# Performance work log

Hardware: AMD Instinct MI355X
Metric: run time of the kernel (lower is better)

## Reference

```python
import jax, jax.numpy as jnp
import numpy as np

N_U, N_P, E = 200000, 50000, 500000
D_U, D_P, H, OUT = 100, 50, 128, 1
BN_EPS = 1e-5


def _lin(k, dout, din):
    s = 1.0 / np.sqrt(din)
    kw, kb = jax.random.split(k)
    W = jax.random.uniform(kw, (dout, din), jnp.float32, -s, s)
    b = jax.random.uniform(kb, (dout,), jnp.float32, -s, s)
    return W, b


def setup_inputs() -> dict:
    key = jax.random.key(0)
    ks = jax.random.split(key, 12)
    x_u = jax.random.normal(ks[0], (N_U, D_U), jnp.float32)
    x_p = jax.random.normal(ks[1], (N_P, D_P), jnp.float32)
    src = jax.random.randint(ks[2], (E,), 0, N_U, jnp.int64) if jax.config.jax_enable_x64 else jax.random.randint(ks[2], (E,), 0, N_U)
    dst = jax.random.randint(ks[3], (E,), N_U, N_U + N_P)
    edge_index = jnp.stack([src, dst]).astype(jnp.int32)
    W_u, b_u = _lin(ks[4], H, D_U)
    W_p, b_p = _lin(ks[5], H, D_P)
    W1l, b1l = _lin(ks[6], H, H)   # SAGEConv lin_l (aggregated neighbors, carries bias)
    W1r, _ = _lin(ks[7], H, H)     # SAGEConv lin_r (root, no bias)
    W2l, b2l = _lin(ks[8], H, H)
    W2r, _ = _lin(ks[9], H, H)
    W_out, b_out = _lin(ks[10], OUT, H)
    return dict(x_u=x_u, x_p=x_p, edge_index=edge_index,
                W_u=W_u, b_u=b_u, W_p=W_p, b_p=b_p,
                W1l=W1l, b1l=b1l, W1r=W1r,
                g1=jnp.ones((H,), jnp.float32), be1=jnp.zeros((H,), jnp.float32),
                W2l=W2l, b2l=b2l, W2r=W2r,
                g2=jnp.ones((H,), jnp.float32), be2=jnp.zeros((H,), jnp.float32),
                W_out=W_out, b_out=b_out)


def reference(x_u, x_p, edge_index, W_u, b_u, W_p, b_p,
              W1l, b1l, W1r, g1, be1, W2l, b2l, W2r, g2, be2,
              W_out, b_out):
    N = x_u.shape[0] + x_p.shape[0]
    # input projections + relu, then concat users/products -> [N, H]
    x = jnp.concatenate([jax.nn.relu(x_u @ W_u.T + b_u),
                         jax.nn.relu(x_p @ W_p.T + b_p)], axis=0)
    # to_undirected: add reversed edges (bipartite => no duplicates)
    src = jnp.concatenate([edge_index[0], edge_index[1]])
    dst = jnp.concatenate([edge_index[1], edge_index[0]])
    deg = jnp.maximum(jax.ops.segment_sum(jnp.ones_like(dst, jnp.float32), dst, num_segments=N), 1.0)

    def sage(h, Wl, bl, Wr):
        # mean aggregation of neighbor features, scatter by dst
        mean = jax.ops.segment_sum(h[src], dst, num_segments=N) / deg[:, None]
        return mean @ Wl.T + bl + h @ Wr.T

    def bn(h, g, b):
        m = h.mean(0)
        v = h.var(0)  # biased variance, as used for normalization in torch BN
        return (h - m) * jax.lax.rsqrt(v + BN_EPS) * g + b

    h1 = jax.nn.relu(bn(sage(x, W1l, b1l, W1r), g1, be1))   # dropout = identity (eval)
    h2 = jax.nn.relu(bn(sage(h1, W2l, b2l, W2r), g2, be2)) + x
    return h2[: x_u.shape[0]] @ W_out.T + b_out
```

## Files before the change

### kernel.cpp

```cpp
#include <hip/hip_runtime.h>
#include <hip/hip_bf16.h>
#include <cstdint>
#include <cstddef>

#define NT   250000
#define NUU  200000
#define NPP  50000
#define EG   500000
#define E2   1000000
#define HD   128
#define NBLK_SCAN 977

#define CNT2_OFF   0ull
#define SPART2_OFF 1000000ull
#define SS2_OFF    1065536ull
#define RPTR2_OFF  1067584ull
#define BSUM2_OFF  2067588ull
#define BMAT2_OFF  2071504ull
#define COL2_OFF   2251728ull
#define X2_OFF     6251728ull
#define R1B_OFF    70251728ull
#define R2B_OFF    134251728ull
#define WS_SPLIT   198251728ull

typedef __hip_bfloat16 bf16;
typedef __attribute__((ext_vector_type(8))) short short8v;
typedef __attribute__((ext_vector_type(4))) float f32x4;

__device__ inline float b2f(short s) { return __builtin_bit_cast(float, ((unsigned)(unsigned short)s) << 16); }
__device__ inline unsigned short f2bf(float f) { return __builtin_bit_cast(unsigned short, __float2bfloat16(f)); }

__global__ __launch_bounds__(256) void k_zero(int* __restrict__ p, int n) {
    for (int i = blockIdx.x * 256 + threadIdx.x; i < n; i += gridDim.x * 256) p[i] = 0;
}

__global__ __launch_bounds__(256) void k_count(const int* __restrict__ ei, int* __restrict__ cnt) {
    for (int e = blockIdx.x * 256 + threadIdx.x; e < E2; e += gridDim.x * 256) {
        int d = (e < EG) ? ei[e + EG] : ei[e - EG];
        atomicAdd(&cnt[d], 1);
    }
}

__global__ __launch_bounds__(256) void k_scan1(const int* __restrict__ cnt, int* __restrict__ bsum) {
    __shared__ int lds[256];
    int i = blockIdx.x * 256 + threadIdx.x;
    int v = (i < NT) ? cnt[i] : 0;
    lds[threadIdx.x] = v; __syncthreads();
    for (int s = 128; s > 0; s >>= 1) {
        if (threadIdx.x < s) lds[threadIdx.x] += lds[threadIdx.x + s];
        __syncthreads();
    }
    if (threadIdx.x == 0) bsum[blockIdx.x] = lds[0];
}

__global__ __launch_bounds__(1024) void k_scan2(int* __restrict__ bsum) {
    __shared__ int lds[1024];
    int i = threadIdx.x;
    int v = (i < NBLK_SCAN) ? bsum[i] : 0;
    lds[i] = v; __syncthreads();
    for (int off = 1; off < 1024; off <<= 1) {
        int t = (i >= off) ? lds[i - off] : 0;
        __syncthreads();
        lds[i] += t;
        __syncthreads();
    }
    if (i < NBLK_SCAN) bsum[i] = lds[i] - v;
}

__global__ __launch_bounds__(256) void k_scan3(const int* __restrict__ cnt, const int* __restrict__ bsum,
                                               int* __restrict__ rp) {
    __shared__ int lds[256];
    int i = blockIdx.x * 256 + threadIdx.x;
    int v = (i < NT) ? cnt[i] : 0;
    lds[threadIdx.x] = v; __syncthreads();
    for (int off = 1; off < 256; off <<= 1) {
        int t = (threadIdx.x >= off) ? lds[threadIdx.x - off] : 0;
        __syncthreads();
        lds[threadIdx.x] += t;
        __syncthreads();
    }
    if (i < NT) rp[i] = bsum[blockIdx.x] + lds[threadIdx.x] - v;
    if (i == 0 && blockIdx.x == 0) rp[NT] = E2;
}

__global__ __launch_bounds__(256) void k_fill(const int* __restrict__ ei, const int* __restrict__ rp,
                                              int* __restrict__ fill, int* __restrict__ col) {
    for (int e = blockIdx.x * 256 + threadIdx.x; e < E2; e += gridDim.x * 256) {
        int s = ei[e];
        int d = (e < EG) ? ei[e + EG] : ei[e - EG];
        int slot = rp[d] + atomicAdd(&fill[d], 1);
        col[slot] = s;
    }
}

__global__ __launch_bounds__(256) void k_wcvt(const float* __restrict__ W1l, const float* __restrict__ W1r,
                                              const float* __restrict__ W2l, const float* __restrict__ W2r,
                                              const float* __restrict__ Wu, const float* __restrict__ Wp,
                                              bf16* __restrict__ B) {
    int i = blockIdx.x * 256 + threadIdx.x;
    if (i < 65536) {
        int layer = i >> 15, rem = i & 32767, o = rem >> 8, k = rem & 255;
        const float* W = layer ? ((k < 128) ? W2l : W2r) : ((k < 128) ? W1l : W1r);
        B[i] = __float2bfloat16(W[o * 128 + (k & 127)]);
    } else if (i < 81920) {
        int rem = i - 65536, o = rem >> 7, k = rem & 127;
        B[i] = __float2bfloat16((k < 100) ? Wu[o * 100 + k] : 0.f);
    } else if (i < 90112) {
        int rem = i - 81920, o = rem >> 6, k = rem & 63;
        B[i] = __float2bfloat16((k < 50) ? Wp[o * 50 + k] : 0.f);
    }
}

template<int DIN, int KPAD>
__global__ __launch_bounds__(256) void k_projm(const float* __restrict__ in, const bf16* __restrict__ Bp,
                                               const float* __restrict__ bias, bf16* __restrict__ outp,
                                               int nrows, int rowbase) {
    __shared__ __align__(16) char As[128 * KPAD * 2];
    const int tid = threadIdx.x;
    const int tb = blockIdx.x * 128;
    constexpr int RSTRIDE = KPAD * 2;
    constexpr int PADE = KPAD - DIN;
    constexpr int PH = PADE / 2;
    constexpr int PPAD = 128 * PH;
    constexpr int PMAIN = 128 * DIN / 2;

    for (int q = tid; q < PPAD; q += 256) {
        int row = q / PH;
        int k = DIN + (q - row * PH) * 2;
        *(unsigned*)(As + row * RSTRIDE + ((((k >> 3) << 4) ^ ((row & 7) << 4)) + (k & 7) * 2)) = 0u;
    }
    for (int q = tid; q < PMAIN; q += 256) {
        int f = q * 2;
        int row = f / DIN, k = f - row * DIN;
        int rg = tb + row; if (rg > nrows - 1) rg = nrows - 1;
        float2 v = *(const float2*)(in + (size_t)rg * DIN + k);
        unsigned u = (unsigned)f2bf(v.x) | ((unsigned)f2bf(v.y) << 16);
        *(unsigned*)(As + row * RSTRIDE + ((((k >> 3) << 4) ^ ((row & 7) << 4)) + (k & 7) * 2)) = u;
    }
    __syncthreads();

    const int lane = tid & 63, wid = tid >> 6;
    const int wr = wid >> 1, wc = wid & 1;
    const int r15 = lane & 15, l4 = lane >> 4;
    constexpr int NKS = KPAD / 32;
    f32x4 acc[4][4] = {};
#pragma unroll
    for (int ks = 0; ks < NKS; ks++) {
        short8v a[4], b[4];
#pragma unroll
        for (int m = 0; m < 4; m++) {
            int rl = wr * 64 + m * 16 + r15;
            a[m] = *(const short8v*)(As + rl * RSTRIDE + ((ks * 64 + l4 * 16) ^ ((rl & 7) << 4)));
        }
#pragma unroll
        for (int n = 0; n < 4; n++) {
            int c = wc * 64 + n * 16 + r15;
            b[n] = *(const short8v*)(Bp + (size_t)c * KPAD + ks * 32 + l4 * 8);
        }
#pragma unroll
        for (int m = 0; m < 4; m++)
#pragma unroll
            for (int n = 0; n < 4; n++)
                acc[m][n] = __builtin_amdgcn_mfma_f32_16x16x32_bf16(a[m], b[n], acc[m][n], 0, 0, 0);
    }
    float bcol[4];
#pragma unroll
    for (int n = 0; n < 4; n++) bcol[n] = bias[wc * 64 + n * 16 + r15];
#pragma unroll
    for (int m = 0; m < 4; m++)
#pragma unroll
        for (int n = 0; n < 4; n++)
#pragma unroll
            for (int g = 0; g < 4; g++) {
                int row = tb + wr * 64 + m * 16 + l4 * 4 + g;
                if (row < nrows) {
                    float v = fmaxf(acc[m][n][g] + bcol[n], 0.f);
                    outp[(size_t)(rowbase + row) * HD + wc * 64 + n * 16 + r15] = __float2bfloat16(v);
                }
            }
}

template<bool NORM>
__global__ __launch_bounds__(256) void k_layer(const bf16* __restrict__ hin, const float* __restrict__ ssv,
                                               const int* __restrict__ rp, const int* __restrict__ col,
                                               const bf16* __restrict__ Bmat, const float* __restrict__ blv,
                                               bf16* __restrict__ outp, float* __restrict__ spart,
                                               int store_n) {
    __shared__ __align__(16) char At[32768];
    __shared__ int rpl[129];
    __shared__ int ctr;
    const int tid = threadIdx.x;
    const int tb = blockIdx.x * 128;

    if (tid < 129) rpl[tid] = rp[min(tb + tid, NT)];
    if (tid == 255) ctr = 0;
    __syncthreads();

    const int lane = tid & 63;
    const int l8 = tid & 7;
    const int fo = l8 * 8;
    float sva[8], tva[8], svb[8], tvb[8];
    if (NORM) {
#pragma unroll
        for (int j = 0; j < 8; j++) {
            sva[j] = ssv[fo + j];      tva[j] = ssv[HD + fo + j];
            svb[j] = ssv[64 + fo + j]; tvb[j] = ssv[HD + 64 + fo + j];
        }
    }
    for (;;) {
        int nl = 0;
        if (l8 == 0) nl = atomicAdd(&ctr, 1);
        nl = __shfl(nl, lane & 56);
        if (nl >= 128) break;
        int s0 = rpl[nl], s1 = rpl[nl + 1];
        float a[8] = {}, b[8] = {};
        for (int p = s0; p < s1; p += 4) {
            int i1 = min(p + 1, s1 - 1), i2 = min(p + 2, s1 - 1), i3 = min(p + 3, s1 - 1);
            int c0 = col[p], c1 = col[i1], c2 = col[i2], c3 = col[i3];
            const bf16* r0p = hin + (size_t)c0 * HD + fo;
            const bf16* r1p = hin + (size_t)c1 * HD + fo;
            const bf16* r2p = hin + (size_t)c2 * HD + fo;
            const bf16* r3p = hin + (size_t)c3 * HD + fo;
            short8v uA0 = *(const short8v*)r0p, uB0 = *(const short8v*)(r0p + 64);
            short8v uA1 = *(const short8v*)r1p, uB1 = *(const short8v*)(r1p + 64);
            short8v uA2 = *(const short8v*)r2p, uB2 = *(const short8v*)(r2p + 64);
            short8v uA3 = *(const short8v*)r3p, uB3 = *(const short8v*)(r3p + 64);
            float m1 = (p + 1 < s1) ? 1.f : 0.f;
            float m2 = (p + 2 < s1) ? 1.f : 0.f;
            float m3 = (p + 3 < s1) ? 1.f : 0.f;
#pragma unroll
            for (int j = 0; j < 8; j++) {
                float vA0 = b2f(uA0[j]), vA1 = b2f(uA1[j]), vA2 = b2f(uA2[j]), vA3 = b2f(uA3[j]);
                float vB0 = b2f(uB0[j]), vB1 = b2f(uB1[j]), vB2 = b2f(uB2[j]), vB3 = b2f(uB3[j]);
                if (NORM) {
                    vA0 = fmaxf(fmaf(vA0, sva[j], tva[j]), 0.f);
                    vA1 = fmaxf(fmaf(vA1, sva[j], tva[j]), 0.f);
                    vA2 = fmaxf(fmaf(vA2, sva[j], tva[j]), 0.f);
                    vA3 = fmaxf(fmaf(vA3, sva[j], tva[j]), 0.f);
                    vB0 = fmaxf(fmaf(vB0, svb[j], tvb[j]), 0.f);
                    vB1 = fmaxf(fmaf(vB1, svb[j], tvb[j]), 0.f);
                    vB2 = fmaxf(fmaf(vB2, svb[j], tvb[j]), 0.f);
                    vB3 = fmaxf(fmaf(vB3, svb[j], tvb[j]), 0.f);
                }
                a[j] += vA0 + m1 * vA1 + m2 * vA2 + m3 * vA3;
                b[j] += vB0 + m1 * vB1 + m2 * vB2 + m3 * vB3;
            }
        }
        float inv = 1.f / (float)max(s1 - s0, 1);
        short8v wa, wb;
#pragma unroll
        for (int j = 0; j < 8; j++) { wa[j] = (short)f2bf(a[j] * inv); wb[j] = (short)f2bf(b[j] * inv); }
        *(short8v*)(At + nl * 256 + ((l8 * 16) ^ ((nl & 7) << 4))) = wa;
        *(short8v*)(At + nl * 256 + (((8 + l8) * 16) ^ ((nl & 7) << 4))) = wb;
    }

    const int seg = tid & 15, r0 = tid >> 4;
    const int sfo = seg * 8;
    short8v vh[8];
#pragma unroll
    for (int it = 0; it < 8; it++) {
        int row = r0 + it * 16;
        int r = tb + row; if (r > NT - 1) r = NT - 1;
        vh[it] = *(const short8v*)(hin + (size_t)r * HD + sfo);
    }
    __syncthreads();

    const int wid = tid >> 6;
    const int wr = wid >> 1, wc = wid & 1;
    const int r15 = lane & 15, l4 = lane >> 4;
    f32x4 acc[4][4] = {};
#pragma unroll
    for (int ks = 0; ks < 4; ks++) {
        short8v a[4], b[4];
#pragma unroll
        for (int m = 0; m < 4; m++) {
            int rl = wr * 64 + m * 16 + r15;
            a[m] = *(const short8v*)(At + rl * 256 + ((ks * 64 + l4 * 16) ^ ((rl & 7) << 4)));
        }
#pragma unroll
        for (int n = 0; n < 4; n++) {
            int c = wc * 64 + n * 16 + r15;
            b[n] = *(const short8v*)(Bmat + (size_t)c * 256 + ks * 32 + l4 * 8);
        }
#pragma unroll
        for (int m = 0; m < 4; m++)
#pragma unroll
            for (int n = 0; n < 4; n++)
                acc[m][n] = __builtin_amdgcn_mfma_f32_16x16x32_bf16(a[m], b[n], acc[m][n], 0, 0, 0);
    }
    __syncthreads();

    if (NORM) {
        float sv2[8], tv2[8];
#pragma unroll
        for (int j = 0; j < 8; j++) { sv2[j] = ssv[sfo + j]; tv2[j] = ssv[HD + sfo + j]; }
#pragma unroll
        for (int it = 0; it < 8; it++) {
#pragma unroll
            for (int j = 0; j < 8; j++) {
                float f = b2f(vh[it][j]);
                vh[it][j] = (short)f2bf(fmaxf(fmaf(f, sv2[j], tv2[j]), 0.f));
            }
        }
    }
#pragma unroll
    for (int it = 0; it < 8; it++) {
        int row = r0 + it * 16;
        *(short8v*)(At + row * 256 + ((seg * 16) ^ ((row & 7) << 4))) = vh[it];
    }
    __syncthreads();

#pragma unroll
    for (int ks = 0; ks < 4; ks++) {
        short8v a[4], b[4];
#pragma unroll
        for (int m = 0; m < 4; m++) {
            int rl = wr * 64 + m * 16 + r15;
            a[m] = *(const short8v*)(At + rl * 256 + ((ks * 64 + l4 * 16) ^ ((rl & 7) << 4)));
        }
#pragma unroll
        for (int n = 0; n < 4; n++) {
            int c = wc * 64 + n * 16 + r15;
            b[n] = *(const short8v*)(Bmat + (size_t)c * 256 + (ks + 4) * 32 + l4 * 8);
        }
#pragma unroll
        for (int m = 0; m < 4; m++)
#pragma unroll
            for (int n = 0; n < 4; n++)
                acc[m][n] = __builtin_amdgcn_mfma_f32_16x16x32_bf16(a[m], b[n], acc[m][n], 0, 0, 0);
    }

    float bcol[4];
#pragma unroll
    for (int n = 0; n < 4; n++) bcol[n] = blv[wc * 64 + n * 16 + r15];
    float ls[4] = {0.f, 0.f, 0.f, 0.f}, lq[4] = {0.f, 0.f, 0.f, 0.f};
#pragma unroll
    for (int m = 0; m < 4; m++)
#pragma unroll
        for (int n = 0; n < 4; n++)
#pragma unroll
            for (int gg = 0; gg < 4; gg++) {
                int row = tb + wr * 64 + m * 16 + l4 * 4 + gg;
                float v = acc[m][n][gg] + bcol[n];
                if (row < NT) { ls[n] += v; lq[n] += v * v; }
                if (row < store_n)
                    outp[(size_t)row * HD + wc * 64 + n * 16 + r15] = __float2bfloat16(v);
            }
    int part = (blockIdx.x & 31) * 256;
#pragma unroll
    for (int n = 0; n < 4; n++) {
        float s = ls[n], q2 = lq[n];
        s  += __shfl_xor(s, 16);  s  += __shfl_xor(s, 32);
        q2 += __shfl_xor(q2, 16); q2 += __shfl_xor(q2, 32);
        if (l4 == 0) {
            atomicAdd(&spart[part + wc * 64 + n * 16 + r15], s);
            atomicAdd(&spart[part + 128 + wc * 64 + n * 16 + r15], q2);
        }
    }
}

__global__ void k_fin(const float* __restrict__ sp, const float* __restrict__ g,
                      const float* __restrict__ be, float* __restrict__ ssout) {
    int j = threadIdx.x;
    float m = 0.f, q = 0.f;
    for (int i = 0; i < 32; i++) { m += sp[i * 256 + j]; q += sp[i * 256 + 128 + j]; }
    m *= (1.f / (float)NT);
    q = q * (1.f / (float)NT) - m * m;
    float s = g[j] * rsqrtf(q + 1e-5f);
    ssout[j] = s;
    ssout[HD + j] = be[j] - m * s;
}

__global__ __launch_bounds__(256) void k_out(const bf16* __restrict__ r2, const float* __restrict__ ss,
                                             const bf16* __restrict__ x, const float* __restrict__ wout,
                                             const float* __restrict__ bout, float* __restrict__ outp) {
    int lane = threadIdx.x & 63;
    int wv = (blockIdx.x * blockDim.x + threadIdx.x) >> 6;
    int nwv = (gridDim.x * blockDim.x) >> 6;
    int g16 = lane >> 4, l16 = lane & 15;
    int fo = l16 * 8;
    float s8[8], t8[8], w8[8];
#pragma unroll
    for (int j = 0; j < 8; j++) {
        s8[j] = ss[fo + j]; t8[j] = ss[HD + fo + j]; w8[j] = wout[fo + j];
    }
    float bo = bout[0];
    for (int r0 = wv * 4; r0 < NUU; r0 += nwv * 4) {
        int row = r0 + g16;
        short8v a  = *(const short8v*)(r2 + (size_t)row * HD + fo);
        short8v xx = *(const short8v*)(x  + (size_t)row * HD + fo);
        float acc = 0.f;
#pragma unroll
        for (int j = 0; j < 8; j++) {
            float h = fmaxf(fmaf(b2f(a[j]), s8[j], t8[j]), 0.f) + b2f(xx[j]);
            acc += h * w8[j];
        }
        acc += __shfl_xor(acc, 1);
        acc += __shfl_xor(acc, 2);
        acc += __shfl_xor(acc, 4);
        acc += __shfl_xor(acc, 8);
        if (l16 == 0) outp[row] = acc + bo;
    }
}

extern "C" void kernel_launch(void* const* d_in, const int* in_sizes, int n_in,
                              void* d_out, int out_size, void* d_ws, size_t ws_size,
                              hipStream_t stream) {
    const float* x_u = (const float*)d_in[0];
    const float* x_p = (const float*)d_in[1];
    const int*   ei  = (const int*)d_in[2];
    const float* W_u = (const float*)d_in[3];
    const float* b_u = (const float*)d_in[4];
    const float* W_p = (const float*)d_in[5];
    const float* b_p = (const float*)d_in[6];
    const float* W1l = (const float*)d_in[7];
    const float* b1l = (const float*)d_in[8];
    const float* W1r = (const float*)d_in[9];
    const float* g1  = (const float*)d_in[10];
    const float* be1 = (const float*)d_in[11];
    const float* W2l = (const float*)d_in[12];
    const float* b2l = (const float*)d_in[13];
    const float* W2r = (const float*)d_in[14];
    const float* g2  = (const float*)d_in[15];
    const float* be2 = (const float*)d_in[16];
    const float* Wout = (const float*)d_in[17];
    const float* bout = (const float*)d_in[18];
    float* out = (float*)d_out;
    char* ws = (char*)d_ws;

    if (ws_size < WS_SPLIT) {
        k_zero<<<512, 256, 0, stream>>>((int*)d_out, out_size);
        return;
    }

    int*  cnt    = (int*)(ws + CNT2_OFF);
    float* spart = (float*)(ws + SPART2_OFF);
    float* ssbuf = (float*)(ws + SS2_OFF);
    int*  rp     = (int*)(ws + RPTR2_OFF);
    int*  bsum   = (int*)(ws + BSUM2_OFF);
    bf16* Bmat   = (bf16*)(ws + BMAT2_OFF);
    int*  col    = (int*)(ws + COL2_OFF);
    bf16* X      = (bf16*)(ws + X2_OFF);
    bf16* R1     = (bf16*)(ws + R1B_OFF);
    bf16* R2     = (bf16*)(ws + R2B_OFF);

    k_zero<<<1043, 256, 0, stream>>>(cnt, 266896);
    k_wcvt<<<352, 256, 0, stream>>>(W1l, W1r, W2l, W2r, W_u, W_p, Bmat);

    k_count<<<1024, 256, 0, stream>>>(ei, cnt);
    k_scan1<<<NBLK_SCAN, 256, 0, stream>>>(cnt, bsum);
    k_scan2<<<1, 1024, 0, stream>>>(bsum);
    k_scan3<<<NBLK_SCAN, 256, 0, stream>>>(cnt, bsum, rp);
    k_zero<<<977, 256, 0, stream>>>(cnt, NT);
    k_fill<<<1024, 256, 0, stream>>>(ei, rp, cnt, col);

    k_projm<100, 128><<<1563, 256, 0, stream>>>(x_u, Bmat + 65536, b_u, X, NUU, 0);
    k_projm<50, 64><<<391, 256, 0, stream>>>(x_p, Bmat + 81920, b_p, X, NPP, NUU);

    k_layer<false><<<1954, 256, 0, stream>>>(X, nullptr, rp, col, Bmat, b1l, R1, spart, NT);
    k_fin<<<1, 128, 0, stream>>>(spart, g1, be1, ssbuf);

    k_layer<true><<<1954, 256, 0, stream>>>(R1, ssbuf, rp, col, Bmat + 32768, b2l, R2, spart + 8192, NUU);
    k_fin<<<1, 128, 0, stream>>>(spart + 8192, g2, be2, ssbuf + 256);

    k_out<<<1024, 256, 0, stream>>>(R2, ssbuf + 256, X, Wout, bout, out);
}
```

Baseline: 435.2 us.

## Merge projection kernels, interleave layer tiles, halve edge loops in CSR build

The count and fill kernels now walk each original edge once and handle both directions, halving the loop trip count and the index loads. The two input-projection launches are merged into one kernel that picks the user or product tile by block index. The SAGE layer kernels remap block IDs so that every fifth block takes a product tile (degree ~20) between four user-node tiles (degree ~2.5), spreading the heavy aggregation tiles across the grid to even out load. k_out gets twice as many blocks. The remap adds a block that exits immediately, and the fill order inside each CSR row changes, which makes the float summation order nondeterministic in a different way.

```diff
diff --git a/kernel.cpp b/kernel.cpp
--- a/kernel.cpp
+++ b/kernel.cpp
@@ -35,9 +35,10 @@
 }
 
 __global__ __launch_bounds__(256) void k_count(const int* __restrict__ ei, int* __restrict__ cnt) {
-    for (int e = blockIdx.x * 256 + threadIdx.x; e < E2; e += gridDim.x * 256) {
-        int d = (e < EG) ? ei[e + EG] : ei[e - EG];
+    for (int e = blockIdx.x * 256 + threadIdx.x; e < EG; e += gridDim.x * 256) {
+        int s = ei[e], d = ei[e + EG];
         atomicAdd(&cnt[d], 1);
+        atomicAdd(&cnt[s], 1);
     }
 }
 
@@ -85,11 +86,12 @@
 
 __global__ __launch_bounds__(256) void k_fill(const int* __restrict__ ei, const int* __restrict__ rp,
                                               int* __restrict__ fill, int* __restrict__ col) {
-    for (int e = blockIdx.x * 256 + threadIdx.x; e < E2; e += gridDim.x * 256) {
-        int s = ei[e];
-        int d = (e < EG) ? ei[e + EG] : ei[e - EG];
-        int slot = rp[d] + atomicAdd(&fill[d], 1);
-        col[slot] = s;
+    for (int e = blockIdx.x * 256 + threadIdx.x; e < EG; e += gridDim.x * 256) {
+        int s = ei[e], d = ei[e + EG];
+        int slot1 = rp[d] + atomicAdd(&fill[d], 1);
+        col[slot1] = s;
+        int slot2 = rp[s] + atomicAdd(&fill[s], 1);
+        col[slot2] = d;
     }
 }
 
@@ -112,12 +114,11 @@
 }
 
 template<int DIN, int KPAD>
-__global__ __launch_bounds__(256) void k_projm(const float* __restrict__ in, const bf16* __restrict__ Bp,
-                                               const float* __restrict__ bias, bf16* __restrict__ outp,
-                                               int nrows, int rowbase) {
-    __shared__ __align__(16) char As[128 * KPAD * 2];
+__device__ __forceinline__ void proj_tile(char* As, const float* __restrict__ in,
+                                          const bf16* __restrict__ Bp, const float* __restrict__ bias,
+                                          bf16* __restrict__ outp, int nrows, int rowbase, int bid) {
     const int tid = threadIdx.x;
-    const int tb = blockIdx.x * 128;
+    const int tb = bid * 128;
     constexpr int RSTRIDE = KPAD * 2;
     constexpr int PADE = KPAD - DIN;
     constexpr int PH = PADE / 2;
@@ -180,17 +181,31 @@
             }
 }
 
+__global__ __launch_bounds__(256) void k_proj2(const float* __restrict__ xu, const float* __restrict__ xp,
+                                               const bf16* __restrict__ Bm, const float* __restrict__ bu,
+                                               const float* __restrict__ bp, bf16* __restrict__ X) {
+    __shared__ __align__(16) char As[32768];
+    if (blockIdx.x < 1563)
+        proj_tile<100, 128>(As, xu, Bm + 65536, bu, X, NUU, 0, blockIdx.x);
+    else
+        proj_tile<50, 64>(As, xp, Bm + 81920, bp, X, NPP, NUU, blockIdx.x - 1563);
+}
+
 template<bool NORM>
 __global__ __launch_bounds__(256) void k_layer(const bf16* __restrict__ hin, const float* __restrict__ ssv,
                                                const int* __restrict__ rp, const int* __restrict__ col,
                                                const bf16* __restrict__ Bmat, const float* __restrict__ blv,
                                                bf16* __restrict__ outp, float* __restrict__ spart,
                                                int store_n) {
+    int g = blockIdx.x / 5, pos = blockIdx.x % 5;
+    int tile = (pos < 4) ? (g * 4 + pos) : (1563 + g);
+    if (pos < 4 && tile > 1562) return;
+
     __shared__ __align__(16) char At[32768];
     __shared__ int rpl[129];
     __shared__ int ctr;
     const int tid = threadIdx.x;
-    const int tb = blockIdx.x * 128;
+    const int tb = tile * 128;
 
     if (tid < 129) rpl[tid] = rp[min(tb + tid, NT)];
     if (tid == 255) ctr = 0;
@@ -346,7 +361,7 @@
                 if (row < store_n)
                     outp[(size_t)row * HD + wc * 64 + n * 16 + r15] = __float2bfloat16(v);
             }
-    int part = (blockIdx.x & 31) * 256;
+    int part = (tile & 31) * 256;
 #pragma unroll
     for (int n = 0; n < 4; n++) {
         float s = ls[n], q2 = lq[n];
@@ -454,14 +469,13 @@
     k_zero<<<977, 256, 0, stream>>>(cnt, NT);
     k_fill<<<1024, 256, 0, stream>>>(ei, rp, cnt, col);
 
-    k_projm<100, 128><<<1563, 256, 0, stream>>>(x_u, Bmat + 65536, b_u, X, NUU, 0);
-    k_projm<50, 64><<<391, 256, 0, stream>>>(x_p, Bmat + 81920, b_p, X, NPP, NUU);
-
-    k_layer<false><<<1954, 256, 0, stream>>>(X, nullptr, rp, col, Bmat, b1l, R1, spart, NT);
+    k_proj2<<<1954, 256, 0, stream>>>(x_u, x_p, Bmat, b_u, b_p, X);
+
+    k_layer<false><<<1955, 256, 0, stream>>>(X, nullptr, rp, col, Bmat, b1l, R1, spart, NT);
     k_fin<<<1, 128, 0, stream>>>(spart, g1, be1, ssbuf);
 
-    k_layer<true><<<1954, 256, 0, stream>>>(R1, ssbuf, rp, col, Bmat + 32768, b2l, R2, spart + 8192, NUU);
+    k_layer<true><<<1955, 256, 0, stream>>>(R1, ssbuf, rp, col, Bmat + 32768, b2l, R2, spart + 8192, NUU);
     k_fin<<<1, 128, 0, stream>>>(spart + 8192, g2, be2, ssbuf + 256);
 
-    k_out<<<1024, 256, 0, stream>>>(R2, ssbuf + 256, X, Wout, bout, out);
-}
+    k_out<<<2048, 256, 0, stream>>>(R2, ssbuf + 256, X, Wout, bout, out);
+}
```

New measurement: 416.2 us. 4.4% less time.
